# Kernel optimization log

Measured on AMD Instinct MI355X. Metric: run time of the kernel, lower is better.

Reference implementation:

```python
import jax, jax.numpy as jnp
import numpy as np

N = 20000   # nodes
E = 320000  # edges
F = 64      # input node features
H = 256     # hidden_layer_size
C = 10      # nbr_classes
G = 64      # graphs in the batch


def _lin(key, fan_in, fan_out):
    k1, k2 = jax.random.split(key)
    bound = 1.0 / np.sqrt(fan_in)
    W = jax.random.uniform(k1, (fan_in, fan_out), jnp.float32, -bound, bound)
    b = jax.random.uniform(k2, (fan_out,), jnp.float32, -bound, bound)
    return W, b


def setup_inputs() -> dict:
    key = jax.random.key(0)
    ks = jax.random.split(key, 10)
    x = jax.random.normal(ks[0], (N, F), jnp.float32)
    edge_index = jax.random.randint(ks[1], (2, E), 0, N)
    batch = jnp.sort(jax.random.randint(ks[2], (N,), 0, G))
    W1, b1 = _lin(ks[3], F, H)
    W2, b2 = _lin(ks[4], H, H)
    W3, b3 = _lin(ks[5], H, H)
    W4, b4 = _lin(ks[6], H, H)
    W5, b5 = _lin(ks[7], H, H)
    Wout, bout = _lin(ks[8], H, C)
    return {"x": x, "edge_index": edge_index, "batch": batch,
            "W1": W1, "b1": b1, "W2": W2, "b2": b2, "W3": W3, "b3": b3,
            "W4": W4, "b4": b4, "W5": W5, "b5": b5, "Wout": Wout, "bout": bout}


def reference(x, edge_index, batch, W1, b1, W2, b2, W3, b3, W4, b4, W5, b5, Wout, bout):
    # GCNConv (Kipf & Welling): add self-loops, D^{-1/2}(A+I)D^{-1/2} (X W) + b.
    # Dropout(p=0.5) is identity in eval mode (reference is deterministic).
    loop = jnp.arange(N)
    row = jnp.concatenate([edge_index[0], loop])  # source nodes, [E+N]
    col = jnp.concatenate([edge_index[1], loop])  # target nodes, [E+N]
    deg = jax.ops.segment_sum(jnp.ones(E + N, x.dtype), col, num_segments=N)
    dinv = jax.lax.rsqrt(deg)  # deg >= 1 thanks to self-loops
    norm = (dinv[row] * dinv[col])[:, None]  # [E+N, 1]

    def gcn_conv(h, W, b):
        m = (h @ W)[row] * norm                      # gather + normalize, [E+N, H]
        return jax.ops.segment_sum(m, col, num_segments=N) + b

    h = x
    for W, b in ((W1, b1), (W2, b2), (W3, b3), (W4, b4), (W5, b5)):
        h = jax.nn.relu(gcn_conv(h, W, b))

    # global_mean_pool over graph ids
    counts = jax.ops.segment_sum(jnp.ones(N, h.dtype), batch, num_segments=G)
    pooled = jax.ops.segment_sum(h, batch, num_segments=G) / jnp.maximum(counts, 1.0)[:, None]
    return pooled @ Wout + bout  # [G, C]
```

## Files before the change

kernel.cpp:

```cpp
#include <hip/hip_runtime.h>

#define NN 20000
#define NE 320000
#define FIN 64
#define HD 256
#define NC 10
#define NG 64
#define NB ((NN + 255) / 256)
#define EBMAX (NE + 15 * NN + 16)

typedef unsigned short u16;
typedef unsigned int u32;
typedef __attribute__((ext_vector_type(8))) short short8;
typedef __attribute__((ext_vector_type(4))) float f32x4;

__device__ __forceinline__ float bf2f(u16 u) {
    union { u32 i; float f; } v; v.i = ((u32)u) << 16; return v.f;
}
__device__ __forceinline__ u16 f2bf(float f) {
    union { float f; u32 i; } v; v.f = f;
    u32 r = v.i + 0x7fffu + ((v.i >> 16) & 1u);
    return (u16)(r >> 16);
}

__global__ void k_deg(const int* __restrict__ col, int* __restrict__ degi,
                      const int* __restrict__ batch, int* __restrict__ gstart) {
    int i = blockIdx.x * 256 + threadIdx.x;
    if (i < NE) atomicAdd(&degi[col[i]], 1);
    if (i < NN) {
        int b = batch[i];
        int prev = (i == 0) ? -1 : batch[i - 1];
        if (b != prev) gstart[b] = i;
    }
}

__global__ void k_pad(u32* __restrict__ ebuf32) {
    int i = blockIdx.x * 256 + threadIdx.x;
    if (i < EBMAX / 2) ebuf32[i] = 0x4E204E20u;
}

__global__ __launch_bounds__(256) void k_scan1(const int* __restrict__ degi,
                                               int* __restrict__ rowptr,
                                               int* __restrict__ bsum) {
    int t = threadIdx.x;
    int i = blockIdx.x * 256 + t;
    int v = (i < NN) ? ((degi[i] + 15) & ~15) : 0;
    int lane = t & 63, wid = t >> 6;
    int x = v;
#pragma unroll
    for (int off = 1; off < 64; off <<= 1) {
        int y = __shfl_up(x, off);
        if (lane >= off) x += y;
    }
    __shared__ int ws[4];
    if (lane == 63) ws[wid] = x;
    __syncthreads();
    int woff = 0;
    for (int w = 0; w < wid; ++w) woff += ws[w];
    if (i < NN) rowptr[i] = woff + x - v;
    if (t == 255) bsum[blockIdx.x] = woff + x;
}

__global__ void k_scan3(const int* __restrict__ degi, const int* __restrict__ bsum,
                        int* __restrict__ rowptr, int* __restrict__ cursor,
                        float* __restrict__ dinv,
                        const float* __restrict__ x, u16* __restrict__ u0) {
    __shared__ int pref[NB];
    if (threadIdx.x < NB) pref[threadIdx.x] = bsum[threadIdx.x];
    __syncthreads();
    if (threadIdx.x == 0) {
        int run = 0;
        for (int k = 0; k < NB; ++k) { int t = pref[k]; pref[k] = run; run += t; }
    }
    __syncthreads();
    int i = blockIdx.x * 256 + threadIdx.x;
    if (i < NN) {
        int dg = degi[i];
        int rp = rowptr[i] + pref[i >> 8];
        rowptr[i] = rp;
        cursor[i] = rp;
        dinv[i] = rsqrtf((float)(1 + dg));
        if (i == NN - 1) rowptr[NN] = rp + ((dg + 15) & ~15);
    }
    if (i < NN * FIN / 4) {
        int node = i >> 4;
        float d = rsqrtf((float)(1 + degi[node]));
        float4 v = *(const float4*)&x[(size_t)i * 4];
        u32 lo = (u32)f2bf(v.x * d) | ((u32)f2bf(v.y * d) << 16);
        u32 hi = (u32)f2bf(v.z * d) | ((u32)f2bf(v.w * d) << 16);
        *(uint2*)&u0[(size_t)i * 4] = make_uint2(lo, hi);
    }
    if (blockIdx.x == 0 && threadIdx.x < FIN) u0[(size_t)NN * FIN + threadIdx.x] = 0;
}

__global__ void k_fill(const int* __restrict__ row, const int* __restrict__ col,
                       int* __restrict__ cursor, u16* __restrict__ ebuf) {
    int e = blockIdx.x * 256 + threadIdx.x;
    if (e < NE) {
        int c = col[e];
        int pos = atomicAdd(&cursor[c], 1);
        ebuf[pos] = (u16)row[e];
    }
}

__global__ __launch_bounds__(256) void k_trans(const float* __restrict__ W0, const float* __restrict__ W1,
                                               const float* __restrict__ W2, const float* __restrict__ W3,
                                               const float* __restrict__ W4,
                                               u16* __restrict__ T0, u16* __restrict__ T1,
                                               u16* __restrict__ T2, u16* __restrict__ T3,
                                               u16* __restrict__ T4) {
    int l = blockIdx.z;
    const float* W = (l == 0) ? W0 : (l == 1) ? W1 : (l == 2) ? W2 : (l == 3) ? W3 : W4;
    u16* T = (l == 0) ? T0 : (l == 1) ? T1 : (l == 2) ? T2 : (l == 3) ? T3 : T4;
    int K = (l == 0) ? FIN : HD;
    int k0 = blockIdx.x * 32;
    if (k0 >= K) return;
    int n0 = blockIdx.y * 32;
    __shared__ float tile[32][33];
    int tx = threadIdx.x & 31, ty = threadIdx.x >> 5;
#pragma unroll
    for (int r = 0; r < 32; r += 8)
        tile[ty + r][tx] = W[(size_t)(k0 + ty + r) * HD + n0 + tx];
    __syncthreads();
#pragma unroll
    for (int r = 0; r < 32; r += 8)
        T[(size_t)(n0 + ty + r) * K + k0 + tx] = f2bf(tile[tx][ty + r]);
}

__global__ __launch_bounds__(256) void k_gatherh(const u16* __restrict__ U,
                                                 const int* __restrict__ rowptr,
                                                 const u16* __restrict__ ebuf,
                                                 const float* __restrict__ dinv,
                                                 u16* __restrict__ Z) {
    int b = blockIdx.x;
    int half = b & 1;
    int tile = b >> 1;
    int n = tile * 4 + (threadIdx.x >> 6);
    if (n >= NN) return;
    int lane = threadIdx.x & 63;
    int grp = lane >> 4;
    int seg = lane & 15;
    int fbase = half * 128 + seg * 8;
    int s = rowptr[n], e = rowptr[n + 1];
    float acc[8];
    if (grp == 0) {
        uint4 v = *(const uint4*)&U[(size_t)n * HD + fbase];
        acc[0] = bf2f((u16)(v.x & 0xffff)); acc[1] = bf2f((u16)(v.x >> 16));
        acc[2] = bf2f((u16)(v.y & 0xffff)); acc[3] = bf2f((u16)(v.y >> 16));
        acc[4] = bf2f((u16)(v.z & 0xffff)); acc[5] = bf2f((u16)(v.z >> 16));
        acc[6] = bf2f((u16)(v.w & 0xffff)); acc[7] = bf2f((u16)(v.w >> 16));
    } else {
#pragma unroll
        for (int k = 0; k < 8; ++k) acc[k] = 0.f;
    }
    for (int j = s; j < e; j += 16) {
        int myid = (lane < 16) ? (int)ebuf[j + lane] : 0;
        uint4 v[4];
#pragma unroll
        for (int k = 0; k < 4; ++k) {
            int r = __shfl(myid, grp * 4 + k);
            v[k] = *(const uint4*)&U[(size_t)r * HD + fbase];
        }
#pragma unroll
        for (int k = 0; k < 4; ++k) {
            acc[0] += bf2f((u16)(v[k].x & 0xffff)); acc[1] += bf2f((u16)(v[k].x >> 16));
            acc[2] += bf2f((u16)(v[k].y & 0xffff)); acc[3] += bf2f((u16)(v[k].y >> 16));
            acc[4] += bf2f((u16)(v[k].z & 0xffff)); acc[5] += bf2f((u16)(v[k].z >> 16));
            acc[6] += bf2f((u16)(v[k].w & 0xffff)); acc[7] += bf2f((u16)(v[k].w >> 16));
        }
    }
#pragma unroll
    for (int k = 0; k < 8; ++k) {
        acc[k] += __shfl_xor(acc[k], 16);
        acc[k] += __shfl_xor(acc[k], 32);
    }
    if (grp == 0) {
        float d = dinv[n];
        uint4 o;
        o.x = (u32)f2bf(acc[0] * d) | ((u32)f2bf(acc[1] * d) << 16);
        o.y = (u32)f2bf(acc[2] * d) | ((u32)f2bf(acc[3] * d) << 16);
        o.z = (u32)f2bf(acc[4] * d) | ((u32)f2bf(acc[5] * d) << 16);
        o.w = (u32)f2bf(acc[6] * d) | ((u32)f2bf(acc[7] * d) << 16);
        *(uint4*)&Z[(size_t)n * HD + fbase] = o;
    }
}

__global__ __launch_bounds__(256) void k_gather64(const u16* __restrict__ U,
                                                  const int* __restrict__ rowptr,
                                                  const u16* __restrict__ ebuf,
                                                  const float* __restrict__ dinv,
                                                  u16* __restrict__ Z) {
    int n = blockIdx.x * 4 + (threadIdx.x >> 6);
    if (n >= NN) return;
    int lane = threadIdx.x & 63;
    int grp = lane >> 3;
    int seg = lane & 7;
    int s = rowptr[n], e = rowptr[n + 1];
    float acc[8];
    if (grp == 0) {
        uint4 v = *(const uint4*)&U[(size_t)n * FIN + seg * 8];
        acc[0] = bf2f((u16)(v.x & 0xffff)); acc[1] = bf2f((u16)(v.x >> 16));
        acc[2] = bf2f((u16)(v.y & 0xffff)); acc[3] = bf2f((u16)(v.y >> 16));
        acc[4] = bf2f((u16)(v.z & 0xffff)); acc[5] = bf2f((u16)(v.z >> 16));
        acc[6] = bf2f((u16)(v.w & 0xffff)); acc[7] = bf2f((u16)(v.w >> 16));
    } else {
#pragma unroll
        for (int k = 0; k < 8; ++k) acc[k] = 0.f;
    }
    for (int j = s; j < e; j += 16) {
        int r0 = (int)ebuf[j + grp];
        int r1 = (int)ebuf[j + 8 + grp];
        uint4 v0 = *(const uint4*)&U[(size_t)r0 * FIN + seg * 8];
        uint4 v1 = *(const uint4*)&U[(size_t)r1 * FIN + seg * 8];
        acc[0] += bf2f((u16)(v0.x & 0xffff)); acc[1] += bf2f((u16)(v0.x >> 16));
        acc[2] += bf2f((u16)(v0.y & 0xffff)); acc[3] += bf2f((u16)(v0.y >> 16));
        acc[4] += bf2f((u16)(v0.z & 0xffff)); acc[5] += bf2f((u16)(v0.z >> 16));
        acc[6] += bf2f((u16)(v0.w & 0xffff)); acc[7] += bf2f((u16)(v0.w >> 16));
        acc[0] += bf2f((u16)(v1.x & 0xffff)); acc[1] += bf2f((u16)(v1.x >> 16));
        acc[2] += bf2f((u16)(v1.y & 0xffff)); acc[3] += bf2f((u16)(v1.y >> 16));
        acc[4] += bf2f((u16)(v1.z & 0xffff)); acc[5] += bf2f((u16)(v1.z >> 16));
        acc[6] += bf2f((u16)(v1.w & 0xffff)); acc[7] += bf2f((u16)(v1.w >> 16));
    }
#pragma unroll
    for (int off = 8; off < 64; off <<= 1)
#pragma unroll
        for (int k = 0; k < 8; ++k) acc[k] += __shfl_xor(acc[k], off);
    if (grp == 0) {
        float d = dinv[n];
        uint4 o;
        o.x = (u32)f2bf(acc[0] * d) | ((u32)f2bf(acc[1] * d) << 16);
        o.y = (u32)f2bf(acc[2] * d) | ((u32)f2bf(acc[3] * d) << 16);
        o.z = (u32)f2bf(acc[4] * d) | ((u32)f2bf(acc[5] * d) << 16);
        o.w = (u32)f2bf(acc[6] * d) | ((u32)f2bf(acc[7] * d) << 16);
        *(uint4*)&Z[(size_t)n * FIN + seg * 8] = o;
    }
}

__global__ __launch_bounds__(256) void k_mm(const u16* __restrict__ A,
                                            const u16* __restrict__ Wt,
                                            const float* __restrict__ bias,
                                            const float* __restrict__ dinv,
                                            u16* __restrict__ O,
                                            int K, int scaleOut) {
    __shared__ u16 Asm[64][40];
    __shared__ u16 Bsm[256][40];
    __shared__ float bs[HD];
    const int m0 = blockIdx.x * 64;
    const int t = threadIdx.x;
    const int wave = t >> 6;
    const int lane = t & 63;
    const int quad = lane >> 4;
    const int l16 = lane & 15;
    const int n0 = wave * 64;
    bs[t] = bias[t];
    if (blockIdx.x == 0) O[(size_t)NN * HD + t] = 0;

    f32x4 acc[4][4];
#pragma unroll
    for (int i = 0; i < 4; ++i)
#pragma unroll
        for (int j = 0; j < 4; ++j) acc[i][j] = (f32x4){0.f, 0.f, 0.f, 0.f};

    for (int k0 = 0; k0 < K; k0 += 32) {
        {
            int row = t >> 2, seg = t & 3;
            int gm = m0 + row;
            float4 v = make_float4(0.f, 0.f, 0.f, 0.f);
            if (gm < NN) v = *(const float4*)&A[(size_t)gm * K + k0 + seg * 8];
            *(float4*)&Asm[row][seg * 8] = v;
        }
        {
#pragma unroll
            for (int j = 0; j < 4; ++j) {
                float4 v = *(const float4*)&Wt[(size_t)t * K + k0 + j * 8];
                *(float4*)&Bsm[t][j * 8] = v;
            }
        }
        __syncthreads();
        short8 a[4], b[4];
#pragma unroll
        for (int i = 0; i < 4; ++i) a[i] = *(const short8*)&Asm[i * 16 + l16][quad * 8];
#pragma unroll
        for (int j = 0; j < 4; ++j) b[j] = *(const short8*)&Bsm[n0 + j * 16 + l16][quad * 8];
#pragma unroll
        for (int i = 0; i < 4; ++i)
#pragma unroll
            for (int j = 0; j < 4; ++j)
                acc[i][j] = __builtin_amdgcn_mfma_f32_16x16x32_bf16(a[i], b[j], acc[i][j], 0, 0, 0);
        __syncthreads();
    }
#pragma unroll
    for (int i = 0; i < 4; ++i) {
#pragma unroll
        for (int r = 0; r < 4; ++r) {
            int m = m0 + i * 16 + quad * 4 + r;
            if (m >= NN) continue;
            float d = scaleOut ? dinv[m] : 1.0f;
#pragma unroll
            for (int j = 0; j < 4; ++j) {
                int n = n0 + j * 16 + l16;
                float val = fmaxf(acc[i][j][r] + bs[n], 0.f) * d;
                O[(size_t)m * HD + n] = f2bf(val);
            }
        }
    }
}

__global__ __launch_bounds__(256) void k_poolout(const u16* __restrict__ h,
                                                 const int* __restrict__ gstart,
                                                 const float* __restrict__ Wout,
                                                 const float* __restrict__ bout,
                                                 float* __restrict__ out) {
    int g = blockIdx.x;
    int t = threadIdx.x;
    __shared__ float pooled[HD];
    __shared__ float part[NC][16];
    __shared__ int s_se[2];
    if (t == 0) {
        int st = gstart[g];
        int en = NN;
        for (int gg = g + 1; gg < NG; ++gg) en = min(en, gstart[gg]);
        s_se[0] = st; s_se[1] = en;
    }
    __syncthreads();
    int st = s_se[0], en = s_se[1];
    float a0 = 0.f, a1 = 0.f, a2 = 0.f, a3 = 0.f;
    int n = st;
    for (; n + 4 <= en; n += 4) {
        a0 += bf2f(h[(size_t)n * HD + t]);
        a1 += bf2f(h[(size_t)(n + 1) * HD + t]);
        a2 += bf2f(h[(size_t)(n + 2) * HD + t]);
        a3 += bf2f(h[(size_t)(n + 3) * HD + t]);
    }
    for (; n < en; ++n) a0 += bf2f(h[(size_t)n * HD + t]);
    float inv = 1.0f / (float)max(en - st, 1);
    pooled[t] = (a0 + a1 + a2 + a3) * inv;
    __syncthreads();
    if (t < NC * 16) {
        int c = t >> 4, l16 = t & 15;
        float s = 0.f;
        for (int f = l16; f < HD; f += 16)
            s = fmaf(pooled[f], Wout[(size_t)f * NC + c], s);
        part[c][l16] = s;
    }
    __syncthreads();
    if (t < NC) {
        float s = 0.f;
#pragma unroll
        for (int k = 0; k < 16; ++k) s += part[t][k];
        out[(size_t)g * NC + t] = s + bout[t];
    }
}

extern "C" void kernel_launch(void* const* d_in, const int* in_sizes, int n_in,
                              void* d_out, int out_size, void* d_ws, size_t ws_size,
                              hipStream_t stream) {
    const float* x     = (const float*)d_in[0];
    const int*   ei    = (const int*)d_in[1];
    const int*   batch = (const int*)d_in[2];
    const float* Wl[5] = {(const float*)d_in[3], (const float*)d_in[5], (const float*)d_in[7],
                          (const float*)d_in[9], (const float*)d_in[11]};
    const float* bl[5] = {(const float*)d_in[4], (const float*)d_in[6], (const float*)d_in[8],
                          (const float*)d_in[10], (const float*)d_in[12]};
    const float* Wout = (const float*)d_in[13];
    const float* bout = (const float*)d_in[14];
    float* out = (float*)d_out;

    const int* row = ei;
    const int* col = ei + NE;

    char* p = (char*)d_ws;
    auto take = [&](size_t bytes) { char* q = p; p += (bytes + 255) & ~(size_t)255; return q; };
    float* dinv   = (float*)take(NN * 4);
    int*   degi   = (int*)take(NN * 4);
    int*   rowptr = (int*)take((NN + 1) * 4);
    int*   cursor = (int*)take(NN * 4);
    int*   bsum   = (int*)take(NB * 4);
    u16*   ebuf   = (u16*)take(EBMAX * 2);
    int*   gstart = (int*)take(NG * 4);
    u16*   Wt[5];
    for (int l = 0; l < 5; ++l) Wt[l] = (u16*)take((size_t)HD * HD * 2);
    u16*   B1     = (u16*)take((size_t)(NN + 1) * HD * 2);
    u16*   B2     = (u16*)take((size_t)(NN + 1) * HD * 2);

    hipMemsetAsync(degi, 0, NN * 4, stream);
    hipMemsetAsync(gstart, 0x7F, NG * 4, stream);
    k_deg<<<(NE + 255) / 256, 256, 0, stream>>>(col, degi, batch, gstart);
    k_pad<<<(EBMAX / 2 + 255) / 256, 256, 0, stream>>>((u32*)ebuf);
    k_scan1<<<NB, 256, 0, stream>>>(degi, rowptr, bsum);
    k_scan3<<<(NN * FIN / 4 + 255) / 256, 256, 0, stream>>>(degi, bsum, rowptr, cursor, dinv, x, B1);
    k_fill<<<(NE + 255) / 256, 256, 0, stream>>>(row, col, cursor, ebuf);
    dim3 tGrid(8, 8, 5);
    k_trans<<<tGrid, 256, 0, stream>>>(Wl[0], Wl[1], Wl[2], Wl[3], Wl[4],
                                       Wt[0], Wt[1], Wt[2], Wt[3], Wt[4]);

    k_gather64<<<(NN + 3) / 4, 256, 0, stream>>>(B1, rowptr, ebuf, dinv, B2);
    k_mm<<<(NN + 63) / 64, 256, 0, stream>>>(B2, Wt[0], bl[0], dinv, B1, FIN, 1);
    const int gGrid = 2 * ((NN + 3) / 4);
    for (int l = 1; l < 5; ++l) {
        k_gatherh<<<gGrid, 256, 0, stream>>>(B1, rowptr, ebuf, dinv, B2);
        k_mm<<<(NN + 63) / 64, 256, 0, stream>>>(B2, Wt[l], bl[l], dinv, B1, HD, (l < 4) ? 1 : 0);
    }

    k_poolout<<<NG, 256, 0, stream>>>(B1, gstart, Wout, bout, out);
}
```

Measured before the change: 348.6 us.

## Fuse neighbor aggregation into GEMM kernel via shared-memory A tile

Merges the per-layer gather and matmul kernels into one kernel. Each block aggregates the neighbors of 32 rows straight into a full-K shared-memory A tile, then runs the MFMA GEMM against streamed weight tiles. This removes the write and re-read of the aggregated intermediate buffer in global memory and halves the kernel launches. In exchange the M tile shrinks from 64 to 32, so each weight tile is reused over fewer rows. The gather phase also has less parallelism per block, and occupancy is set by the launch-bounds hint.

```diff
diff --git a/kernel.cpp b/kernel.cpp
--- a/kernel.cpp
+++ b/kernel.cpp
@@ -127,174 +127,155 @@
         T[(size_t)(n0 + ty + r) * K + k0 + tx] = f2bf(tile[tx][ty + r]);
 }
 
-__global__ __launch_bounds__(256) void k_gatherh(const u16* __restrict__ U,
-                                                 const int* __restrict__ rowptr,
-                                                 const u16* __restrict__ ebuf,
-                                                 const float* __restrict__ dinv,
-                                                 u16* __restrict__ Z) {
-    int b = blockIdx.x;
-    int half = b & 1;
-    int tile = b >> 1;
-    int n = tile * 4 + (threadIdx.x >> 6);
-    if (n >= NN) return;
-    int lane = threadIdx.x & 63;
-    int grp = lane >> 4;
-    int seg = lane & 15;
-    int fbase = half * 128 + seg * 8;
-    int s = rowptr[n], e = rowptr[n + 1];
-    float acc[8];
-    if (grp == 0) {
-        uint4 v = *(const uint4*)&U[(size_t)n * HD + fbase];
-        acc[0] = bf2f((u16)(v.x & 0xffff)); acc[1] = bf2f((u16)(v.x >> 16));
-        acc[2] = bf2f((u16)(v.y & 0xffff)); acc[3] = bf2f((u16)(v.y >> 16));
-        acc[4] = bf2f((u16)(v.z & 0xffff)); acc[5] = bf2f((u16)(v.z >> 16));
-        acc[6] = bf2f((u16)(v.w & 0xffff)); acc[7] = bf2f((u16)(v.w >> 16));
-    } else {
-#pragma unroll
-        for (int k = 0; k < 8; ++k) acc[k] = 0.f;
-    }
-    for (int j = s; j < e; j += 16) {
-        int myid = (lane < 16) ? (int)ebuf[j + lane] : 0;
-        uint4 v[4];
-#pragma unroll
-        for (int k = 0; k < 4; ++k) {
-            int r = __shfl(myid, grp * 4 + k);
-            v[k] = *(const uint4*)&U[(size_t)r * HD + fbase];
-        }
-#pragma unroll
-        for (int k = 0; k < 4; ++k) {
-            acc[0] += bf2f((u16)(v[k].x & 0xffff)); acc[1] += bf2f((u16)(v[k].x >> 16));
-            acc[2] += bf2f((u16)(v[k].y & 0xffff)); acc[3] += bf2f((u16)(v[k].y >> 16));
-            acc[4] += bf2f((u16)(v[k].z & 0xffff)); acc[5] += bf2f((u16)(v[k].z >> 16));
-            acc[6] += bf2f((u16)(v[k].w & 0xffff)); acc[7] += bf2f((u16)(v[k].w >> 16));
-        }
-    }
-#pragma unroll
-    for (int k = 0; k < 8; ++k) {
-        acc[k] += __shfl_xor(acc[k], 16);
-        acc[k] += __shfl_xor(acc[k], 32);
-    }
-    if (grp == 0) {
-        float d = dinv[n];
-        uint4 o;
-        o.x = (u32)f2bf(acc[0] * d) | ((u32)f2bf(acc[1] * d) << 16);
-        o.y = (u32)f2bf(acc[2] * d) | ((u32)f2bf(acc[3] * d) << 16);
-        o.z = (u32)f2bf(acc[4] * d) | ((u32)f2bf(acc[5] * d) << 16);
-        o.w = (u32)f2bf(acc[6] * d) | ((u32)f2bf(acc[7] * d) << 16);
-        *(uint4*)&Z[(size_t)n * HD + fbase] = o;
-    }
-}
-
-__global__ __launch_bounds__(256) void k_gather64(const u16* __restrict__ U,
+__global__ __launch_bounds__(256, 3) void k_fused(const u16* __restrict__ U,
                                                   const int* __restrict__ rowptr,
                                                   const u16* __restrict__ ebuf,
                                                   const float* __restrict__ dinv,
-                                                  u16* __restrict__ Z) {
-    int n = blockIdx.x * 4 + (threadIdx.x >> 6);
-    if (n >= NN) return;
-    int lane = threadIdx.x & 63;
-    int grp = lane >> 3;
-    int seg = lane & 7;
-    int s = rowptr[n], e = rowptr[n + 1];
-    float acc[8];
-    if (grp == 0) {
-        uint4 v = *(const uint4*)&U[(size_t)n * FIN + seg * 8];
-        acc[0] = bf2f((u16)(v.x & 0xffff)); acc[1] = bf2f((u16)(v.x >> 16));
-        acc[2] = bf2f((u16)(v.y & 0xffff)); acc[3] = bf2f((u16)(v.y >> 16));
-        acc[4] = bf2f((u16)(v.z & 0xffff)); acc[5] = bf2f((u16)(v.z >> 16));
-        acc[6] = bf2f((u16)(v.w & 0xffff)); acc[7] = bf2f((u16)(v.w >> 16));
-    } else {
-#pragma unroll
-        for (int k = 0; k < 8; ++k) acc[k] = 0.f;
-    }
-    for (int j = s; j < e; j += 16) {
-        int r0 = (int)ebuf[j + grp];
-        int r1 = (int)ebuf[j + 8 + grp];
-        uint4 v0 = *(const uint4*)&U[(size_t)r0 * FIN + seg * 8];
-        uint4 v1 = *(const uint4*)&U[(size_t)r1 * FIN + seg * 8];
-        acc[0] += bf2f((u16)(v0.x & 0xffff)); acc[1] += bf2f((u16)(v0.x >> 16));
-        acc[2] += bf2f((u16)(v0.y & 0xffff)); acc[3] += bf2f((u16)(v0.y >> 16));
-        acc[4] += bf2f((u16)(v0.z & 0xffff)); acc[5] += bf2f((u16)(v0.z >> 16));
-        acc[6] += bf2f((u16)(v0.w & 0xffff)); acc[7] += bf2f((u16)(v0.w >> 16));
-        acc[0] += bf2f((u16)(v1.x & 0xffff)); acc[1] += bf2f((u16)(v1.x >> 16));
-        acc[2] += bf2f((u16)(v1.y & 0xffff)); acc[3] += bf2f((u16)(v1.y >> 16));
-        acc[4] += bf2f((u16)(v1.z & 0xffff)); acc[5] += bf2f((u16)(v1.z >> 16));
-        acc[6] += bf2f((u16)(v1.w & 0xffff)); acc[7] += bf2f((u16)(v1.w >> 16));
-    }
-#pragma unroll
-    for (int off = 8; off < 64; off <<= 1)
-#pragma unroll
-        for (int k = 0; k < 8; ++k) acc[k] += __shfl_xor(acc[k], off);
-    if (grp == 0) {
-        float d = dinv[n];
-        uint4 o;
-        o.x = (u32)f2bf(acc[0] * d) | ((u32)f2bf(acc[1] * d) << 16);
-        o.y = (u32)f2bf(acc[2] * d) | ((u32)f2bf(acc[3] * d) << 16);
-        o.z = (u32)f2bf(acc[4] * d) | ((u32)f2bf(acc[5] * d) << 16);
-        o.w = (u32)f2bf(acc[6] * d) | ((u32)f2bf(acc[7] * d) << 16);
-        *(uint4*)&Z[(size_t)n * FIN + seg * 8] = o;
-    }
-}
-
-__global__ __launch_bounds__(256) void k_mm(const u16* __restrict__ A,
-                                            const u16* __restrict__ Wt,
-                                            const float* __restrict__ bias,
-                                            const float* __restrict__ dinv,
-                                            u16* __restrict__ O,
-                                            int K, int scaleOut) {
-    __shared__ u16 Asm[64][40];
+                                                  const u16* __restrict__ Wt,
+                                                  const float* __restrict__ bias,
+                                                  u16* __restrict__ O,
+                                                  int K, int scaleOut) {
+    __shared__ u16 Asm[32][264];
     __shared__ u16 Bsm[256][40];
     __shared__ float bs[HD];
-    const int m0 = blockIdx.x * 64;
+    const int m0 = blockIdx.x * 32;
     const int t = threadIdx.x;
     const int wave = t >> 6;
     const int lane = t & 63;
+    bs[t] = bias[t];
+    if (blockIdx.x == 0) O[(size_t)NN * HD + t] = 0;
+
+    if (K == HD) {
+        const int grp = lane >> 4;
+        const int seg = lane & 15;
+        for (int task = wave; task < 64; task += 4) {
+            const int row = task >> 1;
+            const int n = m0 + row;
+            const int fbase = (task & 1) * 128 + seg * 8;
+            const int s = rowptr[n], e = rowptr[n + 1];
+            float acc[8];
+            if (grp == 0) {
+                uint4 v = *(const uint4*)&U[(size_t)n * HD + fbase];
+                acc[0] = bf2f((u16)(v.x & 0xffff)); acc[1] = bf2f((u16)(v.x >> 16));
+                acc[2] = bf2f((u16)(v.y & 0xffff)); acc[3] = bf2f((u16)(v.y >> 16));
+                acc[4] = bf2f((u16)(v.z & 0xffff)); acc[5] = bf2f((u16)(v.z >> 16));
+                acc[6] = bf2f((u16)(v.w & 0xffff)); acc[7] = bf2f((u16)(v.w >> 16));
+            } else {
+#pragma unroll
+                for (int k = 0; k < 8; ++k) acc[k] = 0.f;
+            }
+            for (int j = s; j < e; j += 16) {
+                int myid = (lane < 16) ? (int)ebuf[j + lane] : 0;
+                uint4 v[4];
+#pragma unroll
+                for (int k = 0; k < 4; ++k) {
+                    int r = __shfl(myid, grp * 4 + k);
+                    v[k] = *(const uint4*)&U[(size_t)r * HD + fbase];
+                }
+#pragma unroll
+                for (int k = 0; k < 4; ++k) {
+                    acc[0] += bf2f((u16)(v[k].x & 0xffff)); acc[1] += bf2f((u16)(v[k].x >> 16));
+                    acc[2] += bf2f((u16)(v[k].y & 0xffff)); acc[3] += bf2f((u16)(v[k].y >> 16));
+                    acc[4] += bf2f((u16)(v[k].z & 0xffff)); acc[5] += bf2f((u16)(v[k].z >> 16));
+                    acc[6] += bf2f((u16)(v[k].w & 0xffff)); acc[7] += bf2f((u16)(v[k].w >> 16));
+                }
+            }
+#pragma unroll
+            for (int k = 0; k < 8; ++k) {
+                acc[k] += __shfl_xor(acc[k], 16);
+                acc[k] += __shfl_xor(acc[k], 32);
+            }
+            if (grp == 0) {
+                float d = dinv[n];
+                uint4 o;
+                o.x = (u32)f2bf(acc[0] * d) | ((u32)f2bf(acc[1] * d) << 16);
+                o.y = (u32)f2bf(acc[2] * d) | ((u32)f2bf(acc[3] * d) << 16);
+                o.z = (u32)f2bf(acc[4] * d) | ((u32)f2bf(acc[5] * d) << 16);
+                o.w = (u32)f2bf(acc[6] * d) | ((u32)f2bf(acc[7] * d) << 16);
+                *(uint4*)&Asm[row][fbase] = o;
+            }
+        }
+    } else {
+        const int grp = lane >> 3;
+        const int seg = lane & 7;
+        for (int task = wave; task < 32; task += 4) {
+            const int n = m0 + task;
+            const int s = rowptr[n], e = rowptr[n + 1];
+            float acc[8];
+            if (grp == 0) {
+                uint4 v = *(const uint4*)&U[(size_t)n * FIN + seg * 8];
+                acc[0] = bf2f((u16)(v.x & 0xffff)); acc[1] = bf2f((u16)(v.x >> 16));
+                acc[2] = bf2f((u16)(v.y & 0xffff)); acc[3] = bf2f((u16)(v.y >> 16));
+                acc[4] = bf2f((u16)(v.z & 0xffff)); acc[5] = bf2f((u16)(v.z >> 16));
+                acc[6] = bf2f((u16)(v.w & 0xffff)); acc[7] = bf2f((u16)(v.w >> 16));
+            } else {
+#pragma unroll
+                for (int k = 0; k < 8; ++k) acc[k] = 0.f;
+            }
+            for (int j = s; j < e; j += 16) {
+                int r0 = (int)ebuf[j + grp];
+                int r1 = (int)ebuf[j + 8 + grp];
+                uint4 v0 = *(const uint4*)&U[(size_t)r0 * FIN + seg * 8];
+                uint4 v1 = *(const uint4*)&U[(size_t)r1 * FIN + seg * 8];
+                acc[0] += bf2f((u16)(v0.x & 0xffff)); acc[1] += bf2f((u16)(v0.x >> 16));
+                acc[2] += bf2f((u16)(v0.y & 0xffff)); acc[3] += bf2f((u16)(v0.y >> 16));
+                acc[4] += bf2f((u16)(v0.z & 0xffff)); acc[5] += bf2f((u16)(v0.z >> 16));
+                acc[6] += bf2f((u16)(v0.w & 0xffff)); acc[7] += bf2f((u16)(v0.w >> 16));
+                acc[0] += bf2f((u16)(v1.x & 0xffff)); acc[1] += bf2f((u16)(v1.x >> 16));
+                acc[2] += bf2f((u16)(v1.y & 0xffff)); acc[3] += bf2f((u16)(v1.y >> 16));
+                acc[4] += bf2f((u16)(v1.z & 0xffff)); acc[5] += bf2f((u16)(v1.z >> 16));
+                acc[6] += bf2f((u16)(v1.w & 0xffff)); acc[7] += bf2f((u16)(v1.w >> 16));
+            }
+#pragma unroll
+            for (int off = 8; off < 64; off <<= 1)
+#pragma unroll
+                for (int k = 0; k < 8; ++k) acc[k] += __shfl_xor(acc[k], off);
+            if (grp == 0) {
+                float d = dinv[n];
+                uint4 o;
+                o.x = (u32)f2bf(acc[0] * d) | ((u32)f2bf(acc[1] * d) << 16);
+                o.y = (u32)f2bf(acc[2] * d) | ((u32)f2bf(acc[3] * d) << 16);
+                o.z = (u32)f2bf(acc[4] * d) | ((u32)f2bf(acc[5] * d) << 16);
+                o.w = (u32)f2bf(acc[6] * d) | ((u32)f2bf(acc[7] * d) << 16);
+                *(uint4*)&Asm[task][seg * 8] = o;
+            }
+        }
+    }
+    __syncthreads();
+
     const int quad = lane >> 4;
     const int l16 = lane & 15;
     const int n0 = wave * 64;
-    bs[t] = bias[t];
-    if (blockIdx.x == 0) O[(size_t)NN * HD + t] = 0;
-
-    f32x4 acc[4][4];
-#pragma unroll
-    for (int i = 0; i < 4; ++i)
+    f32x4 acc[2][4];
+#pragma unroll
+    for (int i = 0; i < 2; ++i)
 #pragma unroll
         for (int j = 0; j < 4; ++j) acc[i][j] = (f32x4){0.f, 0.f, 0.f, 0.f};
 
     for (int k0 = 0; k0 < K; k0 += 32) {
-        {
-            int row = t >> 2, seg = t & 3;
-            int gm = m0 + row;
-            float4 v = make_float4(0.f, 0.f, 0.f, 0.f);
-            if (gm < NN) v = *(const float4*)&A[(size_t)gm * K + k0 + seg * 8];
-            *(float4*)&Asm[row][seg * 8] = v;
-        }
-        {
-#pragma unroll
-            for (int j = 0; j < 4; ++j) {
-                float4 v = *(const float4*)&Wt[(size_t)t * K + k0 + j * 8];
-                *(float4*)&Bsm[t][j * 8] = v;
-            }
+#pragma unroll
+        for (int j = 0; j < 4; ++j) {
+            float4 v = *(const float4*)&Wt[(size_t)t * K + k0 + j * 8];
+            *(float4*)&Bsm[t][j * 8] = v;
         }
         __syncthreads();
-        short8 a[4], b[4];
-#pragma unroll
-        for (int i = 0; i < 4; ++i) a[i] = *(const short8*)&Asm[i * 16 + l16][quad * 8];
+        short8 a[2], b[4];
+#pragma unroll
+        for (int i = 0; i < 2; ++i) a[i] = *(const short8*)&Asm[i * 16 + l16][k0 + quad * 8];
 #pragma unroll
         for (int j = 0; j < 4; ++j) b[j] = *(const short8*)&Bsm[n0 + j * 16 + l16][quad * 8];
 #pragma unroll
-        for (int i = 0; i < 4; ++i)
+        for (int i = 0; i < 2; ++i)
 #pragma unroll
             for (int j = 0; j < 4; ++j)
                 acc[i][j] = __builtin_amdgcn_mfma_f32_16x16x32_bf16(a[i], b[j], acc[i][j], 0, 0, 0);
         __syncthreads();
     }
 #pragma unroll
-    for (int i = 0; i < 4; ++i) {
+    for (int i = 0; i < 2; ++i) {
 #pragma unroll
         for (int r = 0; r < 4; ++r) {
             int m = m0 + i * 16 + quad * 4 + r;
-            if (m >= NN) continue;
             float d = scaleOut ? dinv[m] : 1.0f;
 #pragma unroll
             for (int j = 0; j < 4; ++j) {
@@ -394,13 +375,12 @@
     k_trans<<<tGrid, 256, 0, stream>>>(Wl[0], Wl[1], Wl[2], Wl[3], Wl[4],
                                        Wt[0], Wt[1], Wt[2], Wt[3], Wt[4]);
 
-    k_gather64<<<(NN + 3) / 4, 256, 0, stream>>>(B1, rowptr, ebuf, dinv, B2);
-    k_mm<<<(NN + 63) / 64, 256, 0, stream>>>(B2, Wt[0], bl[0], dinv, B1, FIN, 1);
-    const int gGrid = 2 * ((NN + 3) / 4);
-    for (int l = 1; l < 5; ++l) {
-        k_gatherh<<<gGrid, 256, 0, stream>>>(B1, rowptr, ebuf, dinv, B2);
-        k_mm<<<(NN + 63) / 64, 256, 0, stream>>>(B2, Wt[l], bl[l], dinv, B1, HD, (l < 4) ? 1 : 0);
-    }
-
-    k_poolout<<<NG, 256, 0, stream>>>(B1, gstart, Wout, bout, out);
-}
+    const int fGrid = NN / 32;
+    k_fused<<<fGrid, 256, 0, stream>>>(B1, rowptr, ebuf, dinv, Wt[0], bl[0], B2, FIN, 1);
+    k_fused<<<fGrid, 256, 0, stream>>>(B2, rowptr, ebuf, dinv, Wt[1], bl[1], B1, HD, 1);
+    k_fused<<<fGrid, 256, 0, stream>>>(B1, rowptr, ebuf, dinv, Wt[2], bl[2], B2, HD, 1);
+    k_fused<<<fGrid, 256, 0, stream>>>(B2, rowptr, ebuf, dinv, Wt[3], bl[3], B1, HD, 1);
+    k_fused<<<fGrid, 256, 0, stream>>>(B1, rowptr, ebuf, dinv, Wt[4], bl[4], B2, HD, 0);
+
+    k_poolout<<<NG, 256, 0, stream>>>(B2, gstart, Wout, bout, out);
+}
```

Result: slower. 395.7 us (+13.5%).

## Split hidden gather into feature quarters, fuse degree/pad kernels, widen pooling

Applied to the files above, without the earlier changes.

Replaces the half-feature hidden-layer gather with a quarter-feature gather. Each wave now covers 64 features of one node with 8 lanes per edge, and each edge id is read directly from the edge buffer instead of being broadcast by shuffle. Gather outputs use nontemporal stores, and the degree-count and edge-buffer padding kernels are merged into one launch. The pooling kernel uses 512 threads, with two halves striding over nodes, to add parallelism per graph. The quarter split reads each edge list four times instead of twice, trading extra index traffic for more parallel waves and shorter per-wave dependency chains.

```diff
diff --git a/kernel.cpp b/kernel.cpp
--- a/kernel.cpp
+++ b/kernel.cpp
@@ -13,6 +13,7 @@
 typedef unsigned int u32;
 typedef __attribute__((ext_vector_type(8))) short short8;
 typedef __attribute__((ext_vector_type(4))) float f32x4;
+typedef __attribute__((ext_vector_type(4))) u32 u32x4;
 
 __device__ __forceinline__ float bf2f(u16 u) {
     union { u32 i; float f; } v; v.i = ((u32)u) << 16; return v.f;
@@ -22,9 +23,16 @@
     u32 r = v.i + 0x7fffu + ((v.i >> 16) & 1u);
     return (u16)(r >> 16);
 }
-
-__global__ void k_deg(const int* __restrict__ col, int* __restrict__ degi,
-                      const int* __restrict__ batch, int* __restrict__ gstart) {
+__device__ __forceinline__ void accum8(float* acc, const uint4& v) {
+    acc[0] += bf2f((u16)(v.x & 0xffff)); acc[1] += bf2f((u16)(v.x >> 16));
+    acc[2] += bf2f((u16)(v.y & 0xffff)); acc[3] += bf2f((u16)(v.y >> 16));
+    acc[4] += bf2f((u16)(v.z & 0xffff)); acc[5] += bf2f((u16)(v.z >> 16));
+    acc[6] += bf2f((u16)(v.w & 0xffff)); acc[7] += bf2f((u16)(v.w >> 16));
+}
+
+__global__ void k_degpad(const int* __restrict__ col, int* __restrict__ degi,
+                         const int* __restrict__ batch, int* __restrict__ gstart,
+                         u32* __restrict__ ebuf32) {
     int i = blockIdx.x * 256 + threadIdx.x;
     if (i < NE) atomicAdd(&degi[col[i]], 1);
     if (i < NN) {
@@ -32,10 +40,6 @@
         int prev = (i == 0) ? -1 : batch[i - 1];
         if (b != prev) gstart[b] = i;
     }
-}
-
-__global__ void k_pad(u32* __restrict__ ebuf32) {
-    int i = blockIdx.x * 256 + threadIdx.x;
     if (i < EBMAX / 2) ebuf32[i] = 0x4E204E20u;
 }
 
@@ -125,64 +129,6 @@
 #pragma unroll
     for (int r = 0; r < 32; r += 8)
         T[(size_t)(n0 + ty + r) * K + k0 + tx] = f2bf(tile[tx][ty + r]);
-}
-
-__global__ __launch_bounds__(256) void k_gatherh(const u16* __restrict__ U,
-                                                 const int* __restrict__ rowptr,
-                                                 const u16* __restrict__ ebuf,
-                                                 const float* __restrict__ dinv,
-                                                 u16* __restrict__ Z) {
-    int b = blockIdx.x;
-    int half = b & 1;
-    int tile = b >> 1;
-    int n = tile * 4 + (threadIdx.x >> 6);
-    if (n >= NN) return;
-    int lane = threadIdx.x & 63;
-    int grp = lane >> 4;
-    int seg = lane & 15;
-    int fbase = half * 128 + seg * 8;
-    int s = rowptr[n], e = rowptr[n + 1];
-    float acc[8];
-    if (grp == 0) {
-        uint4 v = *(const uint4*)&U[(size_t)n * HD + fbase];
-        acc[0] = bf2f((u16)(v.x & 0xffff)); acc[1] = bf2f((u16)(v.x >> 16));
-        acc[2] = bf2f((u16)(v.y & 0xffff)); acc[3] = bf2f((u16)(v.y >> 16));
-        acc[4] = bf2f((u16)(v.z & 0xffff)); acc[5] = bf2f((u16)(v.z >> 16));
-        acc[6] = bf2f((u16)(v.w & 0xffff)); acc[7] = bf2f((u16)(v.w >> 16));
-    } else {
-#pragma unroll
-        for (int k = 0; k < 8; ++k) acc[k] = 0.f;
-    }
-    for (int j = s; j < e; j += 16) {
-        int myid = (lane < 16) ? (int)ebuf[j + lane] : 0;
-        uint4 v[4];
-#pragma unroll
-        for (int k = 0; k < 4; ++k) {
-            int r = __shfl(myid, grp * 4 + k);
-            v[k] = *(const uint4*)&U[(size_t)r * HD + fbase];
-        }
-#pragma unroll
-        for (int k = 0; k < 4; ++k) {
-            acc[0] += bf2f((u16)(v[k].x & 0xffff)); acc[1] += bf2f((u16)(v[k].x >> 16));
-            acc[2] += bf2f((u16)(v[k].y & 0xffff)); acc[3] += bf2f((u16)(v[k].y >> 16));
-            acc[4] += bf2f((u16)(v[k].z & 0xffff)); acc[5] += bf2f((u16)(v[k].z >> 16));
-            acc[6] += bf2f((u16)(v[k].w & 0xffff)); acc[7] += bf2f((u16)(v[k].w >> 16));
-        }
-    }
-#pragma unroll
-    for (int k = 0; k < 8; ++k) {
-        acc[k] += __shfl_xor(acc[k], 16);
-        acc[k] += __shfl_xor(acc[k], 32);
-    }
-    if (grp == 0) {
-        float d = dinv[n];
-        uint4 o;
-        o.x = (u32)f2bf(acc[0] * d) | ((u32)f2bf(acc[1] * d) << 16);
-        o.y = (u32)f2bf(acc[2] * d) | ((u32)f2bf(acc[3] * d) << 16);
-        o.z = (u32)f2bf(acc[4] * d) | ((u32)f2bf(acc[5] * d) << 16);
-        o.w = (u32)f2bf(acc[6] * d) | ((u32)f2bf(acc[7] * d) << 16);
-        *(uint4*)&Z[(size_t)n * HD + fbase] = o;
-    }
 }
 
 __global__ __launch_bounds__(256) void k_gather64(const u16* __restrict__ U,
@@ -212,14 +158,8 @@
         int r1 = (int)ebuf[j + 8 + grp];
         uint4 v0 = *(const uint4*)&U[(size_t)r0 * FIN + seg * 8];
         uint4 v1 = *(const uint4*)&U[(size_t)r1 * FIN + seg * 8];
-        acc[0] += bf2f((u16)(v0.x & 0xffff)); acc[1] += bf2f((u16)(v0.x >> 16));
-        acc[2] += bf2f((u16)(v0.y & 0xffff)); acc[3] += bf2f((u16)(v0.y >> 16));
-        acc[4] += bf2f((u16)(v0.z & 0xffff)); acc[5] += bf2f((u16)(v0.z >> 16));
-        acc[6] += bf2f((u16)(v0.w & 0xffff)); acc[7] += bf2f((u16)(v0.w >> 16));
-        acc[0] += bf2f((u16)(v1.x & 0xffff)); acc[1] += bf2f((u16)(v1.x >> 16));
-        acc[2] += bf2f((u16)(v1.y & 0xffff)); acc[3] += bf2f((u16)(v1.y >> 16));
-        acc[4] += bf2f((u16)(v1.z & 0xffff)); acc[5] += bf2f((u16)(v1.z >> 16));
-        acc[6] += bf2f((u16)(v1.w & 0xffff)); acc[7] += bf2f((u16)(v1.w >> 16));
+        accum8(acc, v0);
+        accum8(acc, v1);
     }
 #pragma unroll
     for (int off = 8; off < 64; off <<= 1)
@@ -227,12 +167,59 @@
         for (int k = 0; k < 8; ++k) acc[k] += __shfl_xor(acc[k], off);
     if (grp == 0) {
         float d = dinv[n];
-        uint4 o;
+        u32x4 o;
         o.x = (u32)f2bf(acc[0] * d) | ((u32)f2bf(acc[1] * d) << 16);
         o.y = (u32)f2bf(acc[2] * d) | ((u32)f2bf(acc[3] * d) << 16);
         o.z = (u32)f2bf(acc[4] * d) | ((u32)f2bf(acc[5] * d) << 16);
         o.w = (u32)f2bf(acc[6] * d) | ((u32)f2bf(acc[7] * d) << 16);
-        *(uint4*)&Z[(size_t)n * FIN + seg * 8] = o;
+        __builtin_nontemporal_store(o, (u32x4*)&Z[(size_t)n * FIN + seg * 8]);
+    }
+}
+
+__global__ __launch_bounds__(256) void k_gatherq(const u16* __restrict__ U,
+                                                 const int* __restrict__ rowptr,
+                                                 const u16* __restrict__ ebuf,
+                                                 const float* __restrict__ dinv,
+                                                 u16* __restrict__ Z) {
+    int bq = blockIdx.x / 5000;
+    int bb = blockIdx.x - bq * 5000;
+    int n = bb * 4 + (threadIdx.x >> 6);
+    int lane = threadIdx.x & 63;
+    int grp = lane >> 3;
+    int seg = lane & 7;
+    int fb = bq * 64 + seg * 8;
+    int s = rowptr[n], e = rowptr[n + 1];
+    float acc[8];
+    if (grp == 0) {
+        uint4 v = *(const uint4*)&U[(size_t)n * HD + fb];
+        acc[0] = bf2f((u16)(v.x & 0xffff)); acc[1] = bf2f((u16)(v.x >> 16));
+        acc[2] = bf2f((u16)(v.y & 0xffff)); acc[3] = bf2f((u16)(v.y >> 16));
+        acc[4] = bf2f((u16)(v.z & 0xffff)); acc[5] = bf2f((u16)(v.z >> 16));
+        acc[6] = bf2f((u16)(v.w & 0xffff)); acc[7] = bf2f((u16)(v.w >> 16));
+    } else {
+#pragma unroll
+        for (int k = 0; k < 8; ++k) acc[k] = 0.f;
+    }
+    for (int j = s; j < e; j += 16) {
+        int r0 = (int)ebuf[j + grp];
+        int r1 = (int)ebuf[j + 8 + grp];
+        uint4 v0 = *(const uint4*)&U[(size_t)r0 * HD + fb];
+        uint4 v1 = *(const uint4*)&U[(size_t)r1 * HD + fb];
+        accum8(acc, v0);
+        accum8(acc, v1);
+    }
+#pragma unroll
+    for (int off = 8; off < 64; off <<= 1)
+#pragma unroll
+        for (int k = 0; k < 8; ++k) acc[k] += __shfl_xor(acc[k], off);
+    if (grp == 0) {
+        float d = dinv[n];
+        u32x4 o;
+        o.x = (u32)f2bf(acc[0] * d) | ((u32)f2bf(acc[1] * d) << 16);
+        o.y = (u32)f2bf(acc[2] * d) | ((u32)f2bf(acc[3] * d) << 16);
+        o.z = (u32)f2bf(acc[4] * d) | ((u32)f2bf(acc[5] * d) << 16);
+        o.w = (u32)f2bf(acc[6] * d) | ((u32)f2bf(acc[7] * d) << 16);
+        __builtin_nontemporal_store(o, (u32x4*)&Z[(size_t)n * HD + fb]);
     }
 }
 
@@ -306,13 +293,16 @@
     }
 }
 
-__global__ __launch_bounds__(256) void k_poolout(const u16* __restrict__ h,
+__global__ __launch_bounds__(512) void k_poolout(const u16* __restrict__ h,
                                                  const int* __restrict__ gstart,
                                                  const float* __restrict__ Wout,
                                                  const float* __restrict__ bout,
                                                  float* __restrict__ out) {
     int g = blockIdx.x;
     int t = threadIdx.x;
+    int f = t & (HD - 1);
+    int half = t >> 8;
+    __shared__ float pp[2][HD];
     __shared__ float pooled[HD];
     __shared__ float part[NC][16];
     __shared__ int s_se[2];
@@ -325,22 +315,26 @@
     __syncthreads();
     int st = s_se[0], en = s_se[1];
     float a0 = 0.f, a1 = 0.f, a2 = 0.f, a3 = 0.f;
-    int n = st;
-    for (; n + 4 <= en; n += 4) {
-        a0 += bf2f(h[(size_t)n * HD + t]);
-        a1 += bf2f(h[(size_t)(n + 1) * HD + t]);
-        a2 += bf2f(h[(size_t)(n + 2) * HD + t]);
-        a3 += bf2f(h[(size_t)(n + 3) * HD + t]);
-    }
-    for (; n < en; ++n) a0 += bf2f(h[(size_t)n * HD + t]);
-    float inv = 1.0f / (float)max(en - st, 1);
-    pooled[t] = (a0 + a1 + a2 + a3) * inv;
+    int n = st + half;
+    for (; n + 6 < en; n += 8) {
+        a0 += bf2f(h[(size_t)n * HD + f]);
+        a1 += bf2f(h[(size_t)(n + 2) * HD + f]);
+        a2 += bf2f(h[(size_t)(n + 4) * HD + f]);
+        a3 += bf2f(h[(size_t)(n + 6) * HD + f]);
+    }
+    for (; n < en; n += 2) a0 += bf2f(h[(size_t)n * HD + f]);
+    pp[half][f] = a0 + a1 + a2 + a3;
+    __syncthreads();
+    if (t < HD) {
+        float inv = 1.0f / (float)max(en - st, 1);
+        pooled[t] = (pp[0][t] + pp[1][t]) * inv;
+    }
     __syncthreads();
     if (t < NC * 16) {
         int c = t >> 4, l16 = t & 15;
         float s = 0.f;
-        for (int f = l16; f < HD; f += 16)
-            s = fmaf(pooled[f], Wout[(size_t)f * NC + c], s);
+        for (int ff = l16; ff < HD; ff += 16)
+            s = fmaf(pooled[ff], Wout[(size_t)ff * NC + c], s);
         part[c][l16] = s;
     }
     __syncthreads();
@@ -385,8 +379,7 @@
 
     hipMemsetAsync(degi, 0, NN * 4, stream);
     hipMemsetAsync(gstart, 0x7F, NG * 4, stream);
-    k_deg<<<(NE + 255) / 256, 256, 0, stream>>>(col, degi, batch, gstart);
-    k_pad<<<(EBMAX / 2 + 255) / 256, 256, 0, stream>>>((u32*)ebuf);
+    k_degpad<<<(NE + 255) / 256, 256, 0, stream>>>(col, degi, batch, gstart, (u32*)ebuf);
     k_scan1<<<NB, 256, 0, stream>>>(degi, rowptr, bsum);
     k_scan3<<<(NN * FIN / 4 + 255) / 256, 256, 0, stream>>>(degi, bsum, rowptr, cursor, dinv, x, B1);
     k_fill<<<(NE + 255) / 256, 256, 0, stream>>>(row, col, cursor, ebuf);
@@ -394,13 +387,13 @@
     k_trans<<<tGrid, 256, 0, stream>>>(Wl[0], Wl[1], Wl[2], Wl[3], Wl[4],
                                        Wt[0], Wt[1], Wt[2], Wt[3], Wt[4]);
 
+    const int mmGrid = (NN + 63) / 64;
     k_gather64<<<(NN + 3) / 4, 256, 0, stream>>>(B1, rowptr, ebuf, dinv, B2);
-    k_mm<<<(NN + 63) / 64, 256, 0, stream>>>(B2, Wt[0], bl[0], dinv, B1, FIN, 1);
-    const int gGrid = 2 * ((NN + 3) / 4);
+    k_mm<<<mmGrid, 256, 0, stream>>>(B2, Wt[0], bl[0], dinv, B1, FIN, 1);
     for (int l = 1; l < 5; ++l) {
-        k_gatherh<<<gGrid, 256, 0, stream>>>(B1, rowptr, ebuf, dinv, B2);
-        k_mm<<<(NN + 63) / 64, 256, 0, stream>>>(B2, Wt[l], bl[l], dinv, B1, HD, (l < 4) ? 1 : 0);
-    }
-
-    k_poolout<<<NG, 256, 0, stream>>>(B1, gstart, Wout, bout, out);
-}
+        k_gatherq<<<4 * 5000, 256, 0, stream>>>(B1, rowptr, ebuf, dinv, B2);
+        k_mm<<<mmGrid, 256, 0, stream>>>(B2, Wt[l], bl[l], dinv, B1, HD, (l < 4) ? 1 : 0);
+    }
+
+    k_poolout<<<NG, 512, 0, stream>>>(B1, gstart, Wout, bout, out);
+}
```

New measurement: 370.6 us. +6.3%, slower.
